# Performance work log

Hardware: AMD Instinct MI355X
Metric: run time of the kernel (lower is better)

The kernel has to match this reference:

```python
import jax, jax.numpy as jnp
import numpy as np

F_DIM = 4096
HID = 256
COR = 32
N_FRAMES = 200
NB = 30
TS = 9  # 4 + 5 time_steps


def _gru(xg, hg, wx, wh, bx, bh):
    # torch.nn.GRU cell math, gates ordered (r, z, n)
    gx = xg @ wx + bx
    gh = hg @ wh + bh
    xr, xz, xn = jnp.split(gx, 3, axis=-1)
    hr, hz, hn = jnp.split(gh, 3, axis=-1)
    r = jax.nn.sigmoid(xr + hr)
    z = jax.nn.sigmoid(xz + hz)
    n = jnp.tanh(xn + r * hn)
    return (1.0 - z) * n + z * hg


def _sattn(h, mask):
    # parameter-free scaled dot-product attention across active tracks
    d = jnp.asarray(h.shape[-1], h.dtype)
    s = (h @ h.T) / jnp.sqrt(d)
    s = jnp.where(mask[None, :], s, -1e9)
    a = jax.nn.softmax(s, axis=-1)
    out = a @ h
    return jnp.where(mask[:, None], out, h)


def setup_inputs() -> dict:
    key = jax.random.key(0)
    ks = jax.random.split(key, 20)
    flow = jax.random.normal(ks[0], (1, N_FRAMES, NB + 1, F_DIM), jnp.float32)
    x = jax.random.normal(ks[1], (1, N_FRAMES, NB + 1, F_DIM), jnp.float32)
    # y: [track_id, x1,y1,x2,y2, label, conf, d0..d5] -> 13 channels
    track = jnp.broadcast_to(jnp.arange(1, NB + 1, dtype=jnp.float32)[None, None, :, None], (1, N_FRAMES, NB, 1))
    coords = jax.random.uniform(ks[2], (1, N_FRAMES, NB, 4), jnp.float32, 0.0, 1000.0)
    label = jnp.round(jax.random.uniform(ks[3], (1, N_FRAMES, NB, 1), jnp.float32))
    conf = jax.random.uniform(ks[4], (1, N_FRAMES, NB, 1), jnp.float32)
    dist = jax.random.normal(ks[5], (1, N_FRAMES, NB, 6), jnp.float32)
    y = jnp.concatenate([track, coords, label, conf, dist], axis=-1)
    toa = jnp.ones((1, 1), jnp.float32)
    s = 0.02
    p = lambda k, shp: s * jax.random.normal(k, shp, jnp.float32)
    return {
        "x": x, "y": y, "toa": toa, "flow": flow,
        "W_rgb": p(ks[6], (F_DIM, HID)), "b_rgb": jnp.zeros((HID,), jnp.float32),
        "W_bb": p(ks[7], (5, HID)), "b_bb": jnp.zeros((HID,), jnp.float32),
        "W_dd": p(ks[8], (6, HID)), "b_dd": jnp.zeros((HID,), jnp.float32),
        "W_proj": p(ks[9], (HID, COR)), "b_proj": jnp.zeros((COR,), jnp.float32),
        "Wx_c": p(ks[10], (COR, 3 * COR)), "Wh_c": p(ks[11], (COR, 3 * COR)),
        "bx_c": jnp.zeros((3 * COR,), jnp.float32), "bh_c": jnp.zeros((3 * COR,), jnp.float32),
        "Wx_g": p(ks[12], (2 * HID, 3 * HID)), "Wh_g": p(ks[13], (HID, 3 * HID)),
        "bx_g": jnp.zeros((3 * HID,), jnp.float32), "bh_g": jnp.zeros((3 * HID,), jnp.float32),
        "W_out": p(ks[14], (2 * HID + COR, 1)), "b_out": jnp.zeros((1,), jnp.float32),
        "W_pbox": p(ks[15], (2 * HID + COR, 4 * TS)), "b_pbox": jnp.zeros((4 * TS,), jnp.float32),
    }


def reference(x, y, toa, flow, W_rgb, b_rgb, W_bb, b_bb, W_dd, b_dd, W_proj, b_proj,
              Wx_c, Wh_c, bx_c, bh_c, Wx_g, Wh_g, bx_g, bh_g, W_out, b_out, W_pbox, b_pbox):
    T = x.shape[1] - TS
    norm = jnp.array([1920.0, 1200.0, 1920.0, 1200.0], y.dtype)
    nb = y[0, :, :, 1:5] / norm                      # (N, 30, 4) normalized boxes
    # future targets: 9 future frames of normalized boxes, flattened -> (T, 30, 36)
    fut = jnp.concatenate([nb[1 + i:1 + i + T] for i in range(TS)], axis=-1)
    flow_f = flow[0, :T]                             # (T, 31, F)
    yf = y[0, :T]                                    # (T, 30, 13)
    nbf = nb[:T]
    act = yf[..., 0] != 0                            # (T, 30) active-track mask

    def step(carry, inp):
        h, hc, bacc, oacc = carry
        ft, yt, nbt, futt, at = inp
        atf = at.astype(h.dtype)
        rgb = jax.nn.relu(ft @ W_rgb + b_rgb)        # (31, H)
        img = jnp.broadcast_to(rgb[0], (NB, rgb.shape[-1]))
        comb = jnp.concatenate([rgb[1:], img], axis=-1)            # (30, 2H)
        bfeat = jax.nn.relu(jnp.concatenate([nbt, yt[:, 6:7]], axis=-1) @ W_bb + b_bb)
        dfeat = jax.nn.relu(yt[:, 7:13] @ W_dd + b_dd)
        xc = dfeat @ W_proj + b_proj
        hc_n = _gru(xc, hc, Wx_c, Wh_c, bx_c, bh_c)  # CorGRU, output_cor = hidden
        h_n = _gru(comb, h, Wx_g, Wh_g, bx_g, bh_g)
        feat = jnp.concatenate([h_n, bfeat, hc_n], axis=-1)        # (30, 2H+32)
        logit = (feat @ W_out + b_out)[:, 0]
        pbox = feat @ W_pbox + b_pbox                # (30, 36)
        d = pbox - futt
        ad = jnp.abs(d)
        sl1 = jnp.mean(jnp.where(ad < 1.0, 0.5 * d * d, ad - 0.5), axis=-1)  # SmoothL1 per box
        bacc = bacc + jnp.sum(sl1 * atf)
        tgt = yt[:, 5]
        bce = jnp.maximum(logit, 0.0) - logit * tgt + jnp.log1p(jnp.exp(-jnp.abs(logit)))
        oacc = oacc + 0.05 * jnp.sum(bce * atf)
        h2 = jnp.where(at[:, None], h_n, h)
        hc2 = jnp.where(at[:, None], hc_n, hc)
        return (_sattn(h2, at), _sattn(hc2, at), bacc, oacc), None

    init = (jnp.zeros((NB, HID), flow.dtype), jnp.zeros((NB, COR), flow.dtype),
            jnp.zeros((), flow.dtype), jnp.zeros((), flow.dtype))
    (h, hc, bbox_l, obj_l), _ = jax.lax.scan(step, init, (flow_f, yf, nbf, fut, act))
    total = obj_l + bbox_l + 0.3 * bbox_l            # object + bbox + inter(0.3*bbox)
    return total
```

## Files before the change

kernel.cpp:

```cpp
#include <hip/hip_runtime.h>
#include <math.h>
#include <stdint.h>

#define T_STEPS 191
#define NB1 31
#define YS 13
#define NBLK 8

typedef short bf8 __attribute__((ext_vector_type(8)));
typedef float f16x __attribute__((ext_vector_type(16)));

#define MFMA32 __builtin_amdgcn_mfma_f32_32x32x16_bf16

__device__ __forceinline__ float sigmoid_(float x) { return 1.f / (1.f + expf(-x)); }

__device__ __forceinline__ unsigned bf16b(float x){
  unsigned u = __float_as_uint(x);
  return (u + 0x7fffu + ((u>>16)&1u)) >> 16;
}
__device__ __forceinline__ float bf16f(unsigned b){ return __uint_as_float(b<<16); }

__device__ __forceinline__ bf8 ldfrag(const unsigned short* p, int slot){
  uint4 u = *reinterpret_cast<const uint4*>(p + slot*8);
  return __builtin_bit_cast(bf8, u);
}
__device__ __forceinline__ bf8 ldg4(const unsigned* p){
  uint4 u = *reinterpret_cast<const uint4*>(p);
  return __builtin_bit_cast(bf8, u);
}
__device__ __forceinline__ bf8 gather8(const unsigned short* fr, int base){
  unsigned w0 = (unsigned)fr[base]    | ((unsigned)fr[base+8]<<16);
  unsigned w1 = (unsigned)fr[base+16] | ((unsigned)fr[base+24]<<16);
  unsigned w2 = (unsigned)fr[base+32] | ((unsigned)fr[base+40]<<16);
  unsigned w3 = (unsigned)fr[base+48] | ((unsigned)fr[base+56]<<16);
  uint4 u; u.x=w0; u.y=w1; u.z=w2; u.w=w3;
  return __builtin_bit_cast(bf8, u);
}
__device__ __forceinline__ f16x zf16(){
  f16x v;
#pragma unroll
  for (int q=0;q<16;++q) v[q]=0.f;
  return v;
}
__device__ __forceinline__ int aslot(int m, int k){
  return ((k>>4)*64 + m + ((k>>3)&1)*32)*8 + (k&7);
}

__device__ __forceinline__ void store_dw_mall_f(float* p, float v) {
    asm volatile("global_store_dword %0, %1, off sc0 sc1"
                 :: "v"((uintptr_t)p), "v"(v) : "memory");
}
__device__ __forceinline__ void store_dw_mall_u(unsigned* p, unsigned v) {
    asm volatile("global_store_dword %0, %1, off sc0 sc1"
                 :: "v"((uintptr_t)p), "v"(v) : "memory");
}
__device__ __forceinline__ void atomic_inc_mall(unsigned* p) {
    asm volatile("global_atomic_add %0, %1, off sc1"
                 :: "v"((uintptr_t)p), "v"(1u) : "memory");
}
__device__ __forceinline__ unsigned load_u32_mall(const unsigned* p) {
    unsigned v;
    asm volatile("global_load_dword %0, %1, off sc0 sc1\n\ts_waitcnt vmcnt(0)"
                 : "=v"(v) : "v"((uintptr_t)p) : "memory");
    return v;
}

template <bool GATHER, bool RELU>
__global__ __launch_bounds__(256) void gemm_tiled(
    const float* __restrict__ A, const float* __restrict__ B,
    const float* __restrict__ bias, float* __restrict__ C,
    int M, int N, int K)
{
    __shared__ float As[16][65];
    __shared__ float Bs[16][65];
    const int tid = threadIdx.x;
    const int tm = tid >> 4, tn = tid & 15;
    const int rowBase = blockIdx.y * 64;
    const int colBase = blockIdx.x * 64;
    float acc[4][4] = {};
    for (int kt = 0; kt < K; kt += 16) {
        #pragma unroll
        for (int l = 0; l < 4; ++l) {
            const int idx = tid + l * 256;
            const int kk = idx & 15, rr = idx >> 4;
            const int row = rowBase + rr;
            float v = 0.f;
            if (row < M) {
                if (GATHER) {
                    const int t = row / 30, i = row - t * 30;
                    const int k = kt + kk;
                    const int src = (k < 256) ? ((t * NB1 + i + 1) * 256 + k)
                                              : (t * NB1 * 256 + (k - 256));
                    v = A[src];
                } else {
                    v = A[(size_t)row * K + kt + kk];
                }
            }
            As[kk][rr] = v;
            const int nn = idx & 63, k2 = idx >> 6;
            Bs[k2][nn] = B[(size_t)(kt + k2) * N + colBase + nn];
        }
        __syncthreads();
        #pragma unroll
        for (int kk = 0; kk < 16; ++kk) {
            float a[4], b[4];
            #pragma unroll
            for (int i = 0; i < 4; ++i) a[i] = As[kk][tm * 4 + i];
            #pragma unroll
            for (int j = 0; j < 4; ++j) b[j] = Bs[kk][tn * 4 + j];
            #pragma unroll
            for (int i = 0; i < 4; ++i)
                #pragma unroll
                for (int j = 0; j < 4; ++j)
                    acc[i][j] = fmaf(a[i], b[j], acc[i][j]);
        }
        __syncthreads();
    }
    #pragma unroll
    for (int i = 0; i < 4; ++i) {
        const int row = rowBase + tm * 4 + i;
        if (row < M) {
            #pragma unroll
            for (int j = 0; j < 4; ++j) {
                const int col = colBase + tn * 4 + j;
                float v = acc[i][j] + bias[col];
                if (RELU) v = fmaxf(v, 0.f);
                C[(size_t)row * N + col] = v;
            }
        }
    }
}

__global__ __launch_bounds__(256) void prep_wg(const float* __restrict__ Whg,
                                               unsigned* __restrict__ wpg)
{
    const int idx = blockIdx.x * 256 + threadIdx.x;
    const int j  = idx & 3;
    const int l  = (idx >> 2) & 63;
    const int kb = (idx >> 8) & 15;
    const int nt = idx >> 12;
    const int g = nt / 3, gate = nt - g * 3;
    const int col = gate * 256 + g * 32 + (l & 31);
    const int k2 = kb * 8 + ((l >> 5) << 2) + j;
    const unsigned lo = bf16b(Whg[(size_t)(2 * k2) * 768 + col]);
    const unsigned hi = bf16b(Whg[(size_t)(2 * k2 + 1) * 768 + col]);
    wpg[idx] = lo | (hi << 16);
}

__global__ __launch_bounds__(256) void prep_hd(const float* __restrict__ Wpbox,
                                               const float* __restrict__ Wout,
                                               unsigned* __restrict__ hdh,
                                               unsigned* __restrict__ hdl)
{
    const int idx = blockIdx.x * 256 + threadIdx.x;
    if (idx >= 9216) return;
    const int j = idx & 3;
    const int l = (idx >> 2) & 63;
    const int kbnt = idx >> 8;
    const int kb = kbnt % 18, nt = kbnt / 18;
    const int d = nt * 32 + (l & 31);
    const int k0 = kb * 16 + ((l >> 5) << 3) + 2 * j;
    float v0 = 0.f, v1 = 0.f;
    if (d < 37) {
        const int r0 = (k0 < 256) ? k0 : 512 + (k0 - 256);
        const int r1 = (k0 + 1 < 256) ? (k0 + 1) : 512 + (k0 + 1 - 256);
        v0 = (d < 36) ? Wpbox[(size_t)r0 * 36 + d] : Wout[r0];
        v1 = (d < 36) ? Wpbox[(size_t)r1 * 36 + d] : Wout[r1];
    }
    const unsigned h0 = bf16b(v0), h1 = bf16b(v1);
    const unsigned l0 = bf16b(v0 - bf16f(h0)), l1 = bf16b(v1 - bf16f(h1));
    hdh[idx] = h0 | (h1 << 16);
    hdl[idx] = l0 | (l1 << 16);
}

__global__ __launch_bounds__(256) void prep_hcw(const float* __restrict__ Whc,
                                                unsigned* __restrict__ hch,
                                                unsigned* __restrict__ hcl)
{
    const int idx = blockIdx.x * 256 + threadIdx.x;
    if (idx >= 1536) return;
    const int j = idx & 3;
    const int l = (idx >> 2) & 63;
    const int kb = (idx >> 8) & 1;
    const int nt = idx >> 9;
    const int col = nt * 32 + (l & 31);
    const int k0 = kb * 16 + ((l >> 5) << 3) + 2 * j;
    const float v0 = Whc[k0 * 96 + col];
    const float v1 = Whc[(k0 + 1) * 96 + col];
    const unsigned h0 = bf16b(v0), h1 = bf16b(v1);
    const unsigned l0 = bf16b(v0 - bf16f(h0)), l1 = bf16b(v1 - bf16f(h1));
    hch[idx] = h0 | (h1 << 16);
    hcl[idx] = l0 | (l1 << 16);
}

__global__ void prep_bias(const float* __restrict__ bxg, const float* __restrict__ bhg,
                          const float* __restrict__ bxc, const float* __restrict__ bhc,
                          float* __restrict__ biasg, float* __restrict__ biasc)
{
    const int t = threadIdx.x;
    if (t < 768) biasg[t] = bxg[t] + (t < 512 ? bhg[t] : 0.f);
    if (t < 96)  biasc[t] = bxc[t] + (t < 64 ? bhc[t] : 0.f);
}

__global__ __launch_bounds__(256) void precomp_kernel(
    const float* __restrict__ y,
    const float* __restrict__ Wbb, const float* __restrict__ bbb,
    const float* __restrict__ Wdd, const float* __restrict__ bdd,
    const float* __restrict__ Wproj, const float* __restrict__ bproj,
    const float* __restrict__ Wxc, const float* __restrict__ biasc,
    const float* __restrict__ Wpbox, const float* __restrict__ bpbox,
    const float* __restrict__ Wout, const float* __restrict__ bout,
    float* __restrict__ gxc, float* __restrict__ pbox_b, float* __restrict__ logit_b)
{
    const int m = blockIdx.x;
    const int tid = threadIdx.x;
    __shared__ float bf[256], df[256], xcs[32], yl[16];
    if (tid < YS) yl[tid] = y[m * YS + tid];
    __syncthreads();
    const float invnorm[4] = {1.f/1920.f, 1.f/1200.f, 1.f/1920.f, 1.f/1200.f};
    {
        float s = bbb[tid];
        s = fmaf(yl[1] * invnorm[0], Wbb[0 * 256 + tid], s);
        s = fmaf(yl[2] * invnorm[1], Wbb[1 * 256 + tid], s);
        s = fmaf(yl[3] * invnorm[2], Wbb[2 * 256 + tid], s);
        s = fmaf(yl[4] * invnorm[3], Wbb[3 * 256 + tid], s);
        s = fmaf(yl[6],              Wbb[4 * 256 + tid], s);
        bf[tid] = fmaxf(s, 0.f);
    }
    {
        float s = bdd[tid];
        #pragma unroll
        for (int k = 0; k < 6; ++k) s = fmaf(yl[7 + k], Wdd[k * 256 + tid], s);
        df[tid] = fmaxf(s, 0.f);
    }
    __syncthreads();
    {
        const int c = tid >> 3, p = tid & 7;
        float s = 0.f;
        for (int k = p; k < 256; k += 8) s = fmaf(df[k], Wproj[k * 32 + c], s);
        s += __shfl_xor(s, 1); s += __shfl_xor(s, 2); s += __shfl_xor(s, 4);
        if (p == 0) xcs[c] = s + bproj[c];
    }
    __syncthreads();
    if (tid < 96) {
        float s = biasc[tid];
        #pragma unroll
        for (int k = 0; k < 32; ++k) s = fmaf(xcs[k], Wxc[k * 96 + tid], s);
        gxc[m * 96 + tid] = s;
    }
    {
        const int d = tid >> 2, p = tid & 3;
        if (d < 37) {
            float s = 0.f;
            if (d < 36) {
                for (int k = p; k < 256; k += 4) s = fmaf(bf[k], Wpbox[(256 + k) * 36 + d], s);
            } else {
                for (int k = p; k < 256; k += 4) s = fmaf(bf[k], Wout[256 + k], s);
            }
            s += __shfl_xor(s, 1); s += __shfl_xor(s, 2);
            if (p == 0) {
                if (d < 36) pbox_b[m * 36 + d] = s + bpbox[d];
                else        logit_b[m] = s + bout[0];
            }
        }
    }
}

__global__ __launch_bounds__(512, 2) void seq8(
    const float* __restrict__ y,
    const float* __restrict__ gxg,
    const float* __restrict__ gxc,
    const float* __restrict__ pbox_b,
    const float* __restrict__ logit_b,
    const unsigned* __restrict__ wpg,
    const unsigned* __restrict__ hdh, const unsigned* __restrict__ hdl,
    const unsigned* __restrict__ hch, const unsigned* __restrict__ hcl,
    const float* __restrict__ bhg,
    const float* __restrict__ bhc,
    unsigned* __restrict__ h2x,
    float* __restrict__ pbx,
    unsigned* __restrict__ bar,
    float* __restrict__ parts)
{
    const int tid = threadIdx.x;
    const int bb = blockIdx.x;
    const int lane = tid & 63, wid = tid >> 6;
    const int half = lane >> 5, ln31 = lane & 31;

    __shared__ __align__(16) unsigned wgl[12288];
    __shared__ __align__(16) unsigned short hA_hi[8192], hA_lo[8192];
    __shared__ __align__(16) unsigned short hnf_hi[1024], hnf_lo[1024];
    __shared__ __align__(16) unsigned short cf_hi[1024],  cf_lo[1024];
    __shared__ __align__(16) unsigned short cnf_hi[1024], cnf_lo[1024];
    __shared__ __align__(16) unsigned short wf_hi[1024],  wf_lo[1024];
    __shared__ __align__(16) unsigned short cwf_hi[1024], cwf_lo[1024];
    __shared__ float exch[6144];
    __shared__ float gxgs[2880];
    __shared__ float gxcs[2880];
    __shared__ float hcst[1056];
    __shared__ float actf[32], bhnl[32], bhcl[32], red[16];

    {
        const unsigned* wsrc = wpg + (size_t)(3 * bb) * 4096;
        for (int i = tid; i < 12288; i += 512) wgl[i] = wsrc[i];
    }
    for (int i = tid; i < 8192; i += 512){ hA_hi[i] = 0; hA_lo[i] = 0; }
    for (int i = tid; i < 1024; i += 512){
        hnf_hi[i]=0; hnf_lo[i]=0; cf_hi[i]=0; cf_lo[i]=0;
        cnf_hi[i]=0; cnf_lo[i]=0; wf_hi[i]=0; wf_lo[i]=0;
        cwf_hi[i]=0; cwf_lo[i]=0;
    }
    for (int i = tid; i < 1056; i += 512) hcst[i] = 0.f;
    if (tid < 32){ bhnl[tid] = bhg[512 + bb*32 + tid]; bhcl[tid] = bhc[64 + tid]; }
    float bacc = 0.f, oacc = 0.f;
    __syncthreads();

    for (int t = 0; t < T_STEPS; ++t) {
        const int m0 = t * 30;
        const int dbuf = t & 1;
        unsigned* h2b = h2x + dbuf * 8192;
        float* pbb = pbx + dbuf * 9600;

        float4 sg0, sg1, sc0v, sc1v;
        const bool hasg = (tid < 360);
        if (hasg){
            { const int i = tid;       const int obj = i/24, r24 = i - obj*24;
              sg0 = *(const float4*)(gxg + (size_t)(m0+obj)*768 + (r24>>3)*256 + bb*32 + (r24&7)*4); }
            { const int i = tid + 360; const int obj = i/24, r24 = i - obj*24;
              sg1 = *(const float4*)(gxg + (size_t)(m0+obj)*768 + (r24>>3)*256 + bb*32 + (r24&7)*4); }
        }
        const bool hasc = (bb == 7) && (tid < 360);
        if (hasc){
            { const int i = tid;       const int obj = i/24, c4 = i - obj*24;
              sc0v = *(const float4*)(gxc + (size_t)(m0+obj)*96 + c4*4); }
            { const int i = tid + 360; const int obj = i/24, c4 = i - obj*24;
              sc1v = *(const float4*)(gxc + (size_t)(m0+obj)*96 + c4*4); }
        }
        if (tid < 32) actf[tid] = (tid < 30 && y[(size_t)(m0+tid)*YS] != 0.f) ? 1.f : 0.f;

        if (wid < 3){
            f16x acc = zf16();
            const unsigned* wb = wgl + wid * 4096;
#pragma unroll 4
            for (int kb = 0; kb < 16; ++kb){
                const bf8 bw = ldg4(wb + (kb*64 + lane)*4);
                const bf8 ah = ldfrag(hA_hi, kb*64 + lane);
                const bf8 al = ldfrag(hA_lo, kb*64 + lane);
                acc = MFMA32(ah, bw, acc, 0,0,0);
                acc = MFMA32(al, bw, acc, 0,0,0);
            }
#pragma unroll
            for (int q = 0; q < 16; ++q){
                const int row = (q&3) + ((q>>2)<<3) + (half<<2);
                exch[wid*1024 + row*32 + ln31] = acc[q];
            }
        } else if (wid < 6 && bb == 7){
            const int g3 = wid - 3;
            f16x acc = zf16();
#pragma unroll
            for (int kb = 0; kb < 2; ++kb){
                const bf8 ah = ldfrag(cf_hi, kb*64 + lane);
                const bf8 al = ldfrag(cf_lo, kb*64 + lane);
                const bf8 wh = ldg4(hch + ((g3*2 + kb)*64 + lane)*4);
                const bf8 wl = ldg4(hcl + ((g3*2 + kb)*64 + lane)*4);
                acc = MFMA32(ah, wh, acc, 0,0,0);
                acc = MFMA32(ah, wl, acc, 0,0,0);
                acc = MFMA32(al, wh, acc, 0,0,0);
            }
#pragma unroll
            for (int q = 0; q < 16; ++q){
                const int row = (q&3) + ((q>>2)<<3) + (half<<2);
                exch[(3+g3)*1024 + row*32 + ln31] = acc[q];
            }
        }
        if (hasg){
            { const int i = tid;       const int obj = i/24, r24 = i - obj*24;
              *(float4*)(gxgs + obj*96 + r24*4) = sg0; }
            { const int i = tid + 360; const int obj = i/24, r24 = i - obj*24;
              *(float4*)(gxgs + obj*96 + r24*4) = sg1; }
        }
        if (hasc){
            { const int i = tid;       const int obj = i/24, c4 = i - obj*24;
              *(float4*)(gxcs + obj*96 + c4*4) = sc0v; }
            { const int i = tid + 360; const int obj = i/24, c4 = i - obj*24;
              *(float4*)(gxcs + obj*96 + c4*4) = sc1v; }
        }
        __syncthreads();

        if (tid < 480){
#pragma unroll
            for (int s = 0; s < 2; ++s){
                const int e = tid*2 + s;
                const int obj = e >> 5, dim = e & 31;
                const float rv = sigmoid_(exch[obj*32 + dim]        + gxgs[obj*96 + dim]);
                const float zv = sigmoid_(exch[1024 + obj*32 + dim] + gxgs[obj*96 + 32 + dim]);
                const float nv = tanhf(gxgs[obj*96 + 64 + dim]
                                       + rv*(exch[2048 + obj*32 + dim] + bhnl[dim]));
                const int sl = aslot(obj, bb*32 + dim);
                const float h = bf16f(hA_hi[sl]) + bf16f(hA_lo[sl]);
                const float hnv = (1.f - zv)*nv + zv*h;
                const float h2 = (actf[obj] > 0.f) ? hnv : h;
                const unsigned hb = bf16b(h2), lb = bf16b(h2 - bf16f(hb));
                store_dw_mall_u(h2b + sl, hb | (lb << 16));
                const int sl2 = aslot(obj, dim);
                const unsigned nh = bf16b(hnv), nl = bf16b(hnv - bf16f(nh));
                hnf_hi[sl2] = (unsigned short)nh; hnf_lo[sl2] = (unsigned short)nl;
            }
            if (bb == 7){
#pragma unroll
                for (int s = 0; s < 2; ++s){
                    const int e = tid*2 + s;
                    const int obj = e >> 5, cd = e & 31;
                    const float rv = sigmoid_(exch[3072 + obj*32 + cd] + gxcs[obj*96 + cd]);
                    const float zv = sigmoid_(exch[4096 + obj*32 + cd] + gxcs[obj*96 + 32 + cd]);
                    const float nv = tanhf(gxcs[obj*96 + 64 + cd]
                                           + rv*(exch[5120 + obj*32 + cd] + bhcl[cd]));
                    const float hc = hcst[obj*33 + cd];
                    const float cnv = (1.f - zv)*nv + zv*hc;
                    const float c2 = (actf[obj] > 0.f) ? cnv : hc;
                    hcst[obj*33 + cd] = c2;
                    const int sl2 = aslot(obj, cd);
                    const unsigned hb = bf16b(c2), lb = bf16b(c2 - bf16f(hb));
                    cf_hi[sl2] = (unsigned short)hb; cf_lo[sl2] = (unsigned short)lb;
                    const unsigned nh = bf16b(cnv), nl = bf16b(cnv - bf16f(nh));
                    cnf_hi[sl2] = (unsigned short)nh; cnf_lo[sl2] = (unsigned short)nl;
                }
            }
        }
        __syncthreads();

        if (wid < 2){
            f16x hp = zf16();
#pragma unroll
            for (int kb = 0; kb < 2; ++kb){
                const bf8 ah = ldfrag(hnf_hi, kb*64 + lane);
                const bf8 al = ldfrag(hnf_lo, kb*64 + lane);
                const int kbg = 2*bb + kb;
                const bf8 wh = ldg4(hdh + ((wid*18 + kbg)*64 + lane)*4);
                const bf8 wl = ldg4(hdl + ((wid*18 + kbg)*64 + lane)*4);
                hp = MFMA32(ah, wh, hp, 0,0,0);
                hp = MFMA32(al, wh, hp, 0,0,0);
                hp = MFMA32(ah, wl, hp, 0,0,0);
            }
            if (bb == 7){
#pragma unroll
                for (int kb = 0; kb < 2; ++kb){
                    const bf8 ah = ldfrag(cnf_hi, kb*64 + lane);
                    const bf8 al = ldfrag(cnf_lo, kb*64 + lane);
                    const bf8 wh = ldg4(hdh + ((wid*18 + 16 + kb)*64 + lane)*4);
                    const bf8 wl = ldg4(hdl + ((wid*18 + 16 + kb)*64 + lane)*4);
                    hp = MFMA32(ah, wh, hp, 0,0,0);
                    hp = MFMA32(al, wh, hp, 0,0,0);
                    hp = MFMA32(ah, wl, hp, 0,0,0);
                }
            }
            const int d = wid*32 + ln31;
            if (d < 37){
#pragma unroll
                for (int q = 0; q < 16; ++q){
                    const int obj = (q&3) + ((q>>2)<<3) + (half<<2);
                    if (obj < 30) store_dw_mall_f(pbb + (obj*40 + d)*8 + bb, hp[q]);
                }
            }
        }

        asm volatile("s_waitcnt vmcnt(0)" ::: "memory");
        __syncthreads();
        if (tid == 0){
            atomic_inc_mall(bar);
            const unsigned tgtc = (unsigned)(NBLK * (t + 1));
            unsigned cur;
            do { asm volatile("s_sleep 1" :::); cur = load_u32_mall(bar); } while (cur < tgtc);
        }
        __syncthreads();

        {
            const int nOb = (bb == 7) ? 2 : 4;
            if (tid < nOb * 37){
                const int oo = tid / 37, d = tid - oo*37;
                const int obj = bb*4 + oo;
                if (actf[obj] > 0.f){
                    const float* pp = pbb + (obj*40 + d)*8;
                    float4 f0, f1;
                    asm volatile("global_load_dwordx4 %0, %2, off sc0 sc1\n\t"
                                 "global_load_dwordx4 %1, %3, off sc0 sc1\n\t"
                                 "s_waitcnt vmcnt(0)"
                                 : "=v"(f0), "=v"(f1)
                                 : "v"((uintptr_t)pp), "v"((uintptr_t)(pp+4)) : "memory");
                    const float sum8 = f0.x+f0.y+f0.z+f0.w + f1.x+f1.y+f1.z+f1.w;
                    const int m = m0 + obj;
                    if (d < 36){
                        const int s4 = d >> 2, cc = d & 3;
                        const float fn = (cc & 1) ? (1.f/1200.f) : (1.f/1920.f);
                        const float fu = y[(size_t)((t+1+s4)*30 + obj)*YS + 1 + cc] * fn;
                        const float df = sum8 + pbox_b[(size_t)m*36 + d] - fu;
                        const float ad = fabsf(df);
                        bacc += ((ad < 1.f) ? 0.5f*df*df : ad - 0.5f) * (1.f/36.f);
                    } else {
                        const float l = sum8 + logit_b[m];
                        const float tg = y[(size_t)m*YS + 5];
                        oacc += 0.05f * (fmaxf(l, 0.f) - l*tg + log1pf(expf(-fabsf(l))));
                    }
                }
            }
        }
        {
            unsigned uu[16];
#pragma unroll
            for (int j = 0; j < 16; ++j){
                const unsigned* sp = h2b + tid + j*512;
                asm volatile("global_load_dword %0, %1, off sc0 sc1"
                             : "=v"(uu[j]) : "v"((uintptr_t)sp) : "memory");
            }
            asm volatile("s_waitcnt vmcnt(0)" ::: "memory");
#pragma unroll
            for (int j = 0; j < 16; ++j){
                const int idx = tid + j*512;
                hA_hi[idx] = (unsigned short)(uu[j] & 0xffffu);
                hA_lo[idx] = (unsigned short)(uu[j] >> 16);
            }
        }
        __syncthreads();

        if (wid < 3){
            f16x s = zf16();
#pragma unroll 4
            for (int kb = 0; kb < 16; ++kb){
                const bf8 ah = ldfrag(hA_hi, kb*64 + lane);
                const bf8 al = ldfrag(hA_lo, kb*64 + lane);
                if (wid == 0)      s = MFMA32(ah, ah, s, 0,0,0);
                else if (wid == 1) s = MFMA32(ah, al, s, 0,0,0);
                else               s = MFMA32(al, ah, s, 0,0,0);
            }
#pragma unroll
            for (int q = 0; q < 16; ++q){
                const int row = (q&3) + ((q>>2)<<3) + (half<<2);
                exch[wid*1024 + row*32 + ln31] = s[q];
            }
        } else if (wid == 3 && bb == 7){
            f16x s = zf16();
#pragma unroll
            for (int kb = 0; kb < 2; ++kb){
                const bf8 ah = ldfrag(cf_hi, kb*64 + lane);
                const bf8 al = ldfrag(cf_lo, kb*64 + lane);
                s = MFMA32(ah, ah, s, 0,0,0);
                s = MFMA32(ah, al, s, 0,0,0);
                s = MFMA32(al, ah, s, 0,0,0);
            }
#pragma unroll
            for (int q = 0; q < 16; ++q){
                const int row = (q&3) + ((q>>2)<<3) + (half<<2);
                exch[3072 + row*32 + ln31] = s[q];
            }
        }
        __syncthreads();

        if (wid == 0 && lane < 30){
            float sv[30]; float mx = -1e30f;
#pragma unroll
            for (int j = 0; j < 30; ++j){
                float x = exch[lane*32 + j] + exch[1024 + lane*32 + j] + exch[2048 + lane*32 + j];
                x = (actf[j] > 0.f) ? x * 0.0625f : -1e9f;
                sv[j] = x; mx = fmaxf(mx, x);
            }
            float sum = 0.f;
#pragma unroll
            for (int j = 0; j < 30; ++j){ sv[j] = expf(sv[j] - mx); sum += sv[j]; }
            const float inv = 1.f / sum;
#pragma unroll
            for (int j = 0; j < 32; ++j){
                const float w = (j < 30) ? sv[j]*inv : 0.f;
                const unsigned hb = bf16b(w), lb = bf16b(w - bf16f(hb));
                const int sl = aslot(lane, j);
                wf_hi[sl] = (unsigned short)hb; wf_lo[sl] = (unsigned short)lb;
            }
        } else if (wid == 1 && bb == 7 && lane < 30){
            float sv[30]; float mx = -1e30f;
#pragma unroll
            for (int j = 0; j < 30; ++j){
                float x = exch[3072 + lane*32 + j];
                x = (actf[j] > 0.f) ? x * 0.17677669529663687f : -1e9f;
                sv[j] = x; mx = fmaxf(mx, x);
            }
            float sum = 0.f;
#pragma unroll
            for (int j = 0; j < 30; ++j){ sv[j] = expf(sv[j] - mx); sum += sv[j]; }
            const float inv = 1.f / sum;
#pragma unroll
            for (int j = 0; j < 32; ++j){
                const float w = (j < 30) ? sv[j]*inv : 0.f;
                const unsigned hb = bf16b(w), lb = bf16b(w - bf16f(hb));
                const int sl = aslot(lane, j);
                cwf_hi[sl] = (unsigned short)hb; cwf_lo[sl] = (unsigned short)lb;
            }
        }
        __syncthreads();

        {
            const int dd = wid*32 + ln31;
            f16x ao = zf16();
#pragma unroll
            for (int kb2 = 0; kb2 < 2; ++kb2){
                const bf8 wh = ldfrag(wf_hi, kb2*64 + lane);
                const bf8 wl = ldfrag(wf_lo, kb2*64 + lane);
                const int base = ((dd>>4)*64 + kb2*16 + (half<<3) + ((dd>>3)&1)*32)*8 + (dd&7);
                const bf8 bh = gather8(hA_hi, base);
                const bf8 bl = gather8(hA_lo, base);
                ao = MFMA32(wh, bh, ao, 0,0,0);
                ao = MFMA32(wh, bl, ao, 0,0,0);
                ao = MFMA32(wl, bh, ao, 0,0,0);
            }
#pragma unroll
            for (int q = 0; q < 16; ++q){
                const int obj = (q&3) + ((q>>2)<<3) + (half<<2);
                const int sl = aslot(obj, dd);
                const float h2v = bf16f(hA_hi[sl]) + bf16f(hA_lo[sl]);
                const float v = (actf[obj] > 0.f) ? ao[q] : h2v;
                const unsigned hb = bf16b(v), lb = bf16b(v - bf16f(hb));
                hA_hi[sl] = (unsigned short)hb; hA_lo[sl] = (unsigned short)lb;
            }
        }
        if (bb == 7 && wid == 0){
            f16x co = zf16();
#pragma unroll
            for (int kb2 = 0; kb2 < 2; ++kb2){
                const bf8 wh = ldfrag(cwf_hi, kb2*64 + lane);
                const bf8 wl = ldfrag(cwf_lo, kb2*64 + lane);
                const int base = ((ln31>>4)*64 + kb2*16 + (half<<3) + ((ln31>>3)&1)*32)*8 + (ln31&7);
                const bf8 bh = gather8(cf_hi, base);
                const bf8 bl = gather8(cf_lo, base);
                co = MFMA32(wh, bh, co, 0,0,0);
                co = MFMA32(wh, bl, co, 0,0,0);
                co = MFMA32(wl, bh, co, 0,0,0);
            }
#pragma unroll
            for (int q = 0; q < 16; ++q){
                const int obj = (q&3) + ((q>>2)<<3) + (half<<2);
                const float c2v = hcst[obj*33 + ln31];
                const float v = (actf[obj] > 0.f) ? co[q] : c2v;
                hcst[obj*33 + ln31] = v;
                const int sl = aslot(obj, ln31);
                const unsigned hb = bf16b(v), lb = bf16b(v - bf16f(hb));
                cf_hi[sl] = (unsigned short)hb; cf_lo[sl] = (unsigned short)lb;
            }
        }
        __syncthreads();
    }

#pragma unroll
    for (int o = 1; o < 64; o <<= 1){ bacc += __shfl_xor(bacc, o); oacc += __shfl_xor(oacc, o); }
    if (lane == 0){ red[wid] = bacc; red[8 + wid] = oacc; }
    __syncthreads();
    if (tid == 0){
        float b = 0.f, o = 0.f;
        for (int i = 0; i < 8; ++i){ b += red[i]; o += red[8 + i]; }
        parts[bb] = b; parts[8 + bb] = o;
    }
}

__global__ void reduce_kernel(const float* __restrict__ parts, float* __restrict__ out) {
    if (threadIdx.x == 0) {
        float b = 0.f, o = 0.f;
        for (int i = 0; i < NBLK; ++i) { b += parts[i]; o += parts[8 + i]; }
        out[0] = o + 1.3f * b;
    }
}

extern "C" void kernel_launch(void* const* d_in, const int* in_sizes, int n_in,
                              void* d_out, int out_size, void* d_ws, size_t ws_size,
                              hipStream_t stream) {
    (void)in_sizes; (void)n_in; (void)out_size; (void)ws_size;
    const float* y      = (const float*)d_in[1];
    const float* flow   = (const float*)d_in[3];
    const float* W_rgb  = (const float*)d_in[4];
    const float* b_rgb  = (const float*)d_in[5];
    const float* W_bb   = (const float*)d_in[6];
    const float* b_bb   = (const float*)d_in[7];
    const float* W_dd   = (const float*)d_in[8];
    const float* b_dd   = (const float*)d_in[9];
    const float* W_proj = (const float*)d_in[10];
    const float* b_proj = (const float*)d_in[11];
    const float* Wx_c   = (const float*)d_in[12];
    const float* Wh_c   = (const float*)d_in[13];
    const float* bx_c   = (const float*)d_in[14];
    const float* bh_c   = (const float*)d_in[15];
    const float* Wx_g   = (const float*)d_in[16];
    const float* Wh_g   = (const float*)d_in[17];
    const float* bx_g   = (const float*)d_in[18];
    const float* bh_g   = (const float*)d_in[19];
    const float* W_out  = (const float*)d_in[20];
    const float* b_out  = (const float*)d_in[21];
    const float* W_pbox = (const float*)d_in[22];
    const float* b_pbox = (const float*)d_in[23];
    float* out = (float*)d_out;

    char* ws = (char*)d_ws;
    unsigned* bar = (unsigned*)ws;
    unsigned* h2x = (unsigned*)(ws + 256);
    float* pbx    = (float*)(ws + 256 + 65536);
    float* parts  = (float*)(ws + 256 + 65536 + 76800);
    float* base   = (float*)(ws + 256 + 65536 + 76800 + 64);
    size_t off = 0;
    float* rgb    = base + off; off += (size_t)5921 * 256;
    float* gxg    = base + off; off += (size_t)5730 * 768;
    float* gxc    = base + off; off += (size_t)5730 * 96;
    float* pboxb  = base + off; off += (size_t)5730 * 36;
    float* logitb = base + off; off += 5760;
    float* biasg  = base + off; off += 768;
    float* biasc  = base + off; off += 96;
    unsigned* wpg = (unsigned*)(base + off); off += 98304;
    unsigned* hdh = (unsigned*)(base + off); off += 9216;
    unsigned* hdl = (unsigned*)(base + off); off += 9216;
    unsigned* hch = (unsigned*)(base + off); off += 1536;
    unsigned* hcl = (unsigned*)(base + off); off += 1536;

    (void)hipMemsetAsync(d_ws, 0, 256 + 65536, stream);

    prep_bias<<<1, 768, 0, stream>>>(bx_g, bh_g, bx_c, bh_c, biasg, biasc);
    prep_wg<<<384, 256, 0, stream>>>(Wh_g, wpg);
    prep_hd<<<36, 256, 0, stream>>>(W_pbox, W_out, hdh, hdl);
    prep_hcw<<<6, 256, 0, stream>>>(Wh_c, hch, hcl);

    gemm_tiled<false, true><<<dim3(4, 93), 256, 0, stream>>>(flow, W_rgb, b_rgb, rgb, 5921, 256, 4096);
    gemm_tiled<true, false><<<dim3(12, 90), 256, 0, stream>>>(rgb, Wx_g, biasg, gxg, 5730, 768, 512);
    precomp_kernel<<<5730, 256, 0, stream>>>(y, W_bb, b_bb, W_dd, b_dd, W_proj, b_proj,
                                             Wx_c, biasc, W_pbox, b_pbox, W_out, b_out,
                                             gxc, pboxb, logitb);
    seq8<<<NBLK, 512, 0, stream>>>(y, gxg, gxc, pboxb, logitb, wpg, hdh, hdl, hch, hcl,
                                   bh_g, bh_c, h2x, pbx, bar, parts);
    reduce_kernel<<<1, 64, 0, stream>>>(parts, out);
}
```

Before: 4.662 ms.

## Collapse 8-block recurrent kernel into single workgroup, drop global grid barrier

New measurement: 8.103 ms. +73.8%, slower.

```diff
diff --git a/kernel.cpp b/kernel.cpp
--- a/kernel.cpp
+++ b/kernel.cpp
@@ -5,7 +5,6 @@
 #define T_STEPS 191
 #define NB1 31
 #define YS 13
-#define NBLK 8
 
 typedef short bf8 __attribute__((ext_vector_type(8)));
 typedef float f16x __attribute__((ext_vector_type(16)));
@@ -44,25 +43,6 @@
 }
 __device__ __forceinline__ int aslot(int m, int k){
   return ((k>>4)*64 + m + ((k>>3)&1)*32)*8 + (k&7);
-}
-
-__device__ __forceinline__ void store_dw_mall_f(float* p, float v) {
-    asm volatile("global_store_dword %0, %1, off sc0 sc1"
-                 :: "v"((uintptr_t)p), "v"(v) : "memory");
-}
-__device__ __forceinline__ void store_dw_mall_u(unsigned* p, unsigned v) {
-    asm volatile("global_store_dword %0, %1, off sc0 sc1"
-                 :: "v"((uintptr_t)p), "v"(v) : "memory");
-}
-__device__ __forceinline__ void atomic_inc_mall(unsigned* p) {
-    asm volatile("global_atomic_add %0, %1, off sc1"
-                 :: "v"((uintptr_t)p), "v"(1u) : "memory");
-}
-__device__ __forceinline__ unsigned load_u32_mall(const unsigned* p) {
-    unsigned v;
-    asm volatile("global_load_dword %0, %1, off sc0 sc1\n\ts_waitcnt vmcnt(0)"
-                 : "=v"(v) : "v"((uintptr_t)p) : "memory");
-    return v;
 }
 
 template <bool GATHER, bool RELU>
@@ -266,7 +246,7 @@
     }
 }
 
-__global__ __launch_bounds__(512, 2) void seq8(
+__global__ __launch_bounds__(512, 1) void seq1(
     const float* __restrict__ y,
     const float* __restrict__ gxg,
     const float* __restrict__ gxc,
@@ -277,247 +257,146 @@
     const unsigned* __restrict__ hch, const unsigned* __restrict__ hcl,
     const float* __restrict__ bhg,
     const float* __restrict__ bhc,
-    unsigned* __restrict__ h2x,
-    float* __restrict__ pbx,
-    unsigned* __restrict__ bar,
-    float* __restrict__ parts)
+    float* __restrict__ out)
 {
     const int tid = threadIdx.x;
-    const int bb = blockIdx.x;
     const int lane = tid & 63, wid = tid >> 6;
     const int half = lane >> 5, ln31 = lane & 31;
-
-    __shared__ __align__(16) unsigned wgl[12288];
+    const int dd = wid * 32 + ln31;
+
     __shared__ __align__(16) unsigned short hA_hi[8192], hA_lo[8192];
-    __shared__ __align__(16) unsigned short hnf_hi[1024], hnf_lo[1024];
     __shared__ __align__(16) unsigned short cf_hi[1024],  cf_lo[1024];
-    __shared__ __align__(16) unsigned short cnf_hi[1024], cnf_lo[1024];
     __shared__ __align__(16) unsigned short wf_hi[1024],  wf_lo[1024];
     __shared__ __align__(16) unsigned short cwf_hi[1024], cwf_lo[1024];
-    __shared__ float exch[6144];
-    __shared__ float gxgs[2880];
-    __shared__ float gxcs[2880];
-    __shared__ float hcst[1056];
-    __shared__ float actf[32], bhnl[32], bhcl[32], red[16];
-
-    {
-        const unsigned* wsrc = wpg + (size_t)(3 * bb) * 4096;
-        for (int i = tid; i < 12288; i += 512) wgl[i] = wsrc[i];
-    }
+    __shared__ float exch[4096];
+    __shared__ float pbl[1280];
+    __shared__ float actf[32], red[16];
+
     for (int i = tid; i < 8192; i += 512){ hA_hi[i] = 0; hA_lo[i] = 0; }
     for (int i = tid; i < 1024; i += 512){
-        hnf_hi[i]=0; hnf_lo[i]=0; cf_hi[i]=0; cf_lo[i]=0;
-        cnf_hi[i]=0; cnf_lo[i]=0; wf_hi[i]=0; wf_lo[i]=0;
-        cwf_hi[i]=0; cwf_lo[i]=0;
-    }
-    for (int i = tid; i < 1056; i += 512) hcst[i] = 0.f;
-    if (tid < 32){ bhnl[tid] = bhg[512 + bb*32 + tid]; bhcl[tid] = bhc[64 + tid]; }
+        cf_hi[i]=0; cf_lo[i]=0; wf_hi[i]=0; wf_lo[i]=0; cwf_hi[i]=0; cwf_lo[i]=0;
+    }
+    const float bnd = bhg[512 + dd];
+    const float bnc = bhc[64 + ln31];
+
+    float hreg[16], hcreg[16];
+#pragma unroll
+    for (int q = 0; q < 16; ++q){ hreg[q] = 0.f; hcreg[q] = 0.f; }
     float bacc = 0.f, oacc = 0.f;
+
+    int lobj[3], ldc[3]; bool lval[3];
+#pragma unroll
+    for (int r3 = 0; r3 < 3; ++r3){
+        const int c = (tid - 128) + 384 * r3;
+        lval[r3] = (wid >= 2) && (c >= 0) && (c < 1110);
+        const int cc2 = lval[r3] ? c : 0;
+        lobj[r3] = cc2 / 37; ldc[r3] = cc2 - lobj[r3] * 37;
+    }
     __syncthreads();
 
-    for (int t = 0; t < T_STEPS; ++t) {
+    for (int t = 0; t < T_STEPS; ++t){
         const int m0 = t * 30;
-        const int dbuf = t & 1;
-        unsigned* h2b = h2x + dbuf * 8192;
-        float* pbb = pbx + dbuf * 9600;
-
-        float4 sg0, sg1, sc0v, sc1v;
-        const bool hasg = (tid < 360);
-        if (hasg){
-            { const int i = tid;       const int obj = i/24, r24 = i - obj*24;
-              sg0 = *(const float4*)(gxg + (size_t)(m0+obj)*768 + (r24>>3)*256 + bb*32 + (r24&7)*4); }
-            { const int i = tid + 360; const int obj = i/24, r24 = i - obj*24;
-              sg1 = *(const float4*)(gxg + (size_t)(m0+obj)*768 + (r24>>3)*256 + bb*32 + (r24&7)*4); }
-        }
-        const bool hasc = (bb == 7) && (tid < 360);
-        if (hasc){
-            { const int i = tid;       const int obj = i/24, c4 = i - obj*24;
-              sc0v = *(const float4*)(gxc + (size_t)(m0+obj)*96 + c4*4); }
-            { const int i = tid + 360; const int obj = i/24, c4 = i - obj*24;
-              sc1v = *(const float4*)(gxc + (size_t)(m0+obj)*96 + c4*4); }
-        }
-        if (tid < 32) actf[tid] = (tid < 30 && y[(size_t)(m0+tid)*YS] != 0.f) ? 1.f : 0.f;
-
-        if (wid < 3){
-            f16x acc = zf16();
-            const unsigned* wb = wgl + wid * 4096;
+
+        if (tid < 32) actf[tid] = (tid < 30 && y[(size_t)(m0 + tid) * YS] != 0.f) ? 1.f : 0.f;
+        float gr[16], gz[16], gn[16];
+#pragma unroll
+        for (int q = 0; q < 16; ++q){
+            const int obj = (q&3) + ((q>>2)<<3) + (half<<2);
+            if (obj < 30){
+                const float* gp = gxg + (size_t)(m0 + obj) * 768 + dd;
+                gr[q] = gp[0]; gz[q] = gp[256]; gn[q] = gp[512];
+            } else { gr[q] = 0.f; gz[q] = 0.f; gn[q] = 0.f; }
+        }
+        float pfu[3], ppb[3]; float ptg = 0.f;
+#pragma unroll
+        for (int r3 = 0; r3 < 3; ++r3){
+            pfu[r3] = 0.f; ppb[r3] = 0.f;
+            if (lval[r3]){
+                const int obj = lobj[r3], d = ldc[r3];
+                const int m = m0 + obj;
+                if (d < 36){
+                    const int s4 = d >> 2, cc = d & 3;
+                    const float fn = (cc & 1) ? (1.f/1200.f) : (1.f/1920.f);
+                    pfu[r3] = y[(size_t)((t + 1 + s4)*30 + obj)*YS + 1 + cc] * fn;
+                    ppb[r3] = pbox_b[(size_t)m*36 + d];
+                } else {
+                    ppb[r3] = logit_b[m];
+                    ptg = y[(size_t)m*YS + 5];
+                }
+            }
+        }
+
+        f16x aR = zf16(), aZ = zf16(), aN = zf16();
+        {
+            const unsigned* bRp = wpg + ((size_t)((wid*3 + 0)*16)*64 + lane)*4;
+            const unsigned* bZp = wpg + ((size_t)((wid*3 + 1)*16)*64 + lane)*4;
+            const unsigned* bNp = wpg + ((size_t)((wid*3 + 2)*16)*64 + lane)*4;
 #pragma unroll 4
             for (int kb = 0; kb < 16; ++kb){
-                const bf8 bw = ldg4(wb + (kb*64 + lane)*4);
+                const bf8 br = ldg4(bRp + kb*256);
+                const bf8 bz = ldg4(bZp + kb*256);
+                const bf8 bn = ldg4(bNp + kb*256);
                 const bf8 ah = ldfrag(hA_hi, kb*64 + lane);
                 const bf8 al = ldfrag(hA_lo, kb*64 + lane);
-                acc = MFMA32(ah, bw, acc, 0,0,0);
-                acc = MFMA32(al, bw, acc, 0,0,0);
-            }
-#pragma unroll
-            for (int q = 0; q < 16; ++q){
-                const int row = (q&3) + ((q>>2)<<3) + (half<<2);
-                exch[wid*1024 + row*32 + ln31] = acc[q];
-            }
-        } else if (wid < 6 && bb == 7){
+                aR = MFMA32(ah, br, aR, 0,0,0); aR = MFMA32(al, br, aR, 0,0,0);
+                aZ = MFMA32(ah, bz, aZ, 0,0,0); aZ = MFMA32(al, bz, aZ, 0,0,0);
+                aN = MFMA32(ah, bn, aN, 0,0,0); aN = MFMA32(al, bn, aN, 0,0,0);
+            }
+        }
+        if (wid >= 3 && wid < 6){
             const int g3 = wid - 3;
-            f16x acc = zf16();
+            f16x cacc = zf16();
 #pragma unroll
             for (int kb = 0; kb < 2; ++kb){
                 const bf8 ah = ldfrag(cf_hi, kb*64 + lane);
                 const bf8 al = ldfrag(cf_lo, kb*64 + lane);
                 const bf8 wh = ldg4(hch + ((g3*2 + kb)*64 + lane)*4);
                 const bf8 wl = ldg4(hcl + ((g3*2 + kb)*64 + lane)*4);
-                acc = MFMA32(ah, wh, acc, 0,0,0);
-                acc = MFMA32(ah, wl, acc, 0,0,0);
-                acc = MFMA32(al, wh, acc, 0,0,0);
+                cacc = MFMA32(ah, wh, cacc, 0,0,0);
+                cacc = MFMA32(ah, wl, cacc, 0,0,0);
+                cacc = MFMA32(al, wh, cacc, 0,0,0);
             }
 #pragma unroll
             for (int q = 0; q < 16; ++q){
                 const int row = (q&3) + ((q>>2)<<3) + (half<<2);
-                exch[(3+g3)*1024 + row*32 + ln31] = acc[q];
-            }
-        }
-        if (hasg){
-            { const int i = tid;       const int obj = i/24, r24 = i - obj*24;
-              *(float4*)(gxgs + obj*96 + r24*4) = sg0; }
-            { const int i = tid + 360; const int obj = i/24, r24 = i - obj*24;
-              *(float4*)(gxgs + obj*96 + r24*4) = sg1; }
-        }
-        if (hasc){
-            { const int i = tid;       const int obj = i/24, c4 = i - obj*24;
-              *(float4*)(gxcs + obj*96 + c4*4) = sc0v; }
-            { const int i = tid + 360; const int obj = i/24, c4 = i - obj*24;
-              *(float4*)(gxcs + obj*96 + c4*4) = sc1v; }
+                exch[g3*1024 + row*32 + ln31] = cacc[q];
+            }
         }
         __syncthreads();
 
-        if (tid < 480){
-#pragma unroll
-            for (int s = 0; s < 2; ++s){
-                const int e = tid*2 + s;
-                const int obj = e >> 5, dim = e & 31;
-                const float rv = sigmoid_(exch[obj*32 + dim]        + gxgs[obj*96 + dim]);
-                const float zv = sigmoid_(exch[1024 + obj*32 + dim] + gxgs[obj*96 + 32 + dim]);
-                const float nv = tanhf(gxgs[obj*96 + 64 + dim]
-                                       + rv*(exch[2048 + obj*32 + dim] + bhnl[dim]));
-                const int sl = aslot(obj, bb*32 + dim);
-                const float h = bf16f(hA_hi[sl]) + bf16f(hA_lo[sl]);
-                const float hnv = (1.f - zv)*nv + zv*h;
-                const float h2 = (actf[obj] > 0.f) ? hnv : h;
-                const unsigned hb = bf16b(h2), lb = bf16b(h2 - bf16f(hb));
-                store_dw_mall_u(h2b + sl, hb | (lb << 16));
-                const int sl2 = aslot(obj, dim);
-                const unsigned nh = bf16b(hnv), nl = bf16b(hnv - bf16f(nh));
-                hnf_hi[sl2] = (unsigned short)nh; hnf_lo[sl2] = (unsigned short)nl;
-            }
-            if (bb == 7){
-#pragma unroll
-                for (int s = 0; s < 2; ++s){
-                    const int e = tid*2 + s;
-                    const int obj = e >> 5, cd = e & 31;
-                    const float rv = sigmoid_(exch[3072 + obj*32 + cd] + gxcs[obj*96 + cd]);
-                    const float zv = sigmoid_(exch[4096 + obj*32 + cd] + gxcs[obj*96 + 32 + cd]);
-                    const float nv = tanhf(gxcs[obj*96 + 64 + cd]
-                                           + rv*(exch[5120 + obj*32 + cd] + bhcl[cd]));
-                    const float hc = hcst[obj*33 + cd];
-                    const float cnv = (1.f - zv)*nv + zv*hc;
-                    const float c2 = (actf[obj] > 0.f) ? cnv : hc;
-                    hcst[obj*33 + cd] = c2;
-                    const int sl2 = aslot(obj, cd);
-                    const unsigned hb = bf16b(c2), lb = bf16b(c2 - bf16f(hb));
-                    cf_hi[sl2] = (unsigned short)hb; cf_lo[sl2] = (unsigned short)lb;
-                    const unsigned nh = bf16b(cnv), nl = bf16b(cnv - bf16f(nh));
-                    cnf_hi[sl2] = (unsigned short)nh; cnf_lo[sl2] = (unsigned short)nl;
-                }
-            }
-        }
-        __syncthreads();
-
-        if (wid < 2){
-            f16x hp = zf16();
-#pragma unroll
-            for (int kb = 0; kb < 2; ++kb){
-                const bf8 ah = ldfrag(hnf_hi, kb*64 + lane);
-                const bf8 al = ldfrag(hnf_lo, kb*64 + lane);
-                const int kbg = 2*bb + kb;
-                const bf8 wh = ldg4(hdh + ((wid*18 + kbg)*64 + lane)*4);
-                const bf8 wl = ldg4(hdl + ((wid*18 + kbg)*64 + lane)*4);
-                hp = MFMA32(ah, wh, hp, 0,0,0);
-                hp = MFMA32(al, wh, hp, 0,0,0);
-                hp = MFMA32(ah, wl, hp, 0,0,0);
-            }
-            if (bb == 7){
-#pragma unroll
-                for (int kb = 0; kb < 2; ++kb){
-                    const bf8 ah = ldfrag(cnf_hi, kb*64 + lane);
-                    const bf8 al = ldfrag(cnf_lo, kb*64 + lane);
-                    const bf8 wh = ldg4(hdh + ((wid*18 + 16 + kb)*64 + lane)*4);
-                    const bf8 wl = ldg4(hdl + ((wid*18 + 16 + kb)*64 + lane)*4);
-                    hp = MFMA32(ah, wh, hp, 0,0,0);
-                    hp = MFMA32(al, wh, hp, 0,0,0);
-                    hp = MFMA32(ah, wl, hp, 0,0,0);
-                }
-            }
-            const int d = wid*32 + ln31;
-            if (d < 37){
-#pragma unroll
-                for (int q = 0; q < 16; ++q){
-                    const int obj = (q&3) + ((q>>2)<<3) + (half<<2);
-                    if (obj < 30) store_dw_mall_f(pbb + (obj*40 + d)*8 + bb, hp[q]);
-                }
-            }
-        }
-
-        asm volatile("s_waitcnt vmcnt(0)" ::: "memory");
-        __syncthreads();
-        if (tid == 0){
-            atomic_inc_mall(bar);
-            const unsigned tgtc = (unsigned)(NBLK * (t + 1));
-            unsigned cur;
-            do { asm volatile("s_sleep 1" :::); cur = load_u32_mall(bar); } while (cur < tgtc);
-        }
-        __syncthreads();
-
-        {
-            const int nOb = (bb == 7) ? 2 : 4;
-            if (tid < nOb * 37){
-                const int oo = tid / 37, d = tid - oo*37;
-                const int obj = bb*4 + oo;
-                if (actf[obj] > 0.f){
-                    const float* pp = pbb + (obj*40 + d)*8;
-                    float4 f0, f1;
-                    asm volatile("global_load_dwordx4 %0, %2, off sc0 sc1\n\t"
-                                 "global_load_dwordx4 %1, %3, off sc0 sc1\n\t"
-                                 "s_waitcnt vmcnt(0)"
-                                 : "=v"(f0), "=v"(f1)
-                                 : "v"((uintptr_t)pp), "v"((uintptr_t)(pp+4)) : "memory");
-                    const float sum8 = f0.x+f0.y+f0.z+f0.w + f1.x+f1.y+f1.z+f1.w;
-                    const int m = m0 + obj;
-                    if (d < 36){
-                        const int s4 = d >> 2, cc = d & 3;
-                        const float fn = (cc & 1) ? (1.f/1200.f) : (1.f/1920.f);
-                        const float fu = y[(size_t)((t+1+s4)*30 + obj)*YS + 1 + cc] * fn;
-                        const float df = sum8 + pbox_b[(size_t)m*36 + d] - fu;
-                        const float ad = fabsf(df);
-                        bacc += ((ad < 1.f) ? 0.5f*df*df : ad - 0.5f) * (1.f/36.f);
-                    } else {
-                        const float l = sum8 + logit_b[m];
-                        const float tg = y[(size_t)m*YS + 5];
-                        oacc += 0.05f * (fmaxf(l, 0.f) - l*tg + log1pf(expf(-fabsf(l))));
-                    }
-                }
-            }
-        }
-        {
-            unsigned uu[16];
-#pragma unroll
-            for (int j = 0; j < 16; ++j){
-                const unsigned* sp = h2b + tid + j*512;
-                asm volatile("global_load_dword %0, %1, off sc0 sc1"
-                             : "=v"(uu[j]) : "v"((uintptr_t)sp) : "memory");
-            }
-            asm volatile("s_waitcnt vmcnt(0)" ::: "memory");
-#pragma unroll
-            for (int j = 0; j < 16; ++j){
-                const int idx = tid + j*512;
-                hA_hi[idx] = (unsigned short)(uu[j] & 0xffffu);
-                hA_lo[idx] = (unsigned short)(uu[j] >> 16);
+#pragma unroll
+        for (int q = 0; q < 16; ++q){
+            const int obj = (q&3) + ((q>>2)<<3) + (half<<2);
+            const float rv = sigmoid_(aR[q] + gr[q]);
+            const float zv = sigmoid_(aZ[q] + gz[q]);
+            const float nv = tanhf(gn[q] + rv*(aN[q] + bnd));
+            const float hv = hreg[q];
+            const float hnv = (1.f - zv)*nv + zv*hv;
+            const float h2 = (actf[obj] > 0.f) ? hnv : hv;
+            hreg[q] = h2;
+            const int sl = aslot(obj, dd);
+            const unsigned hb = bf16b(h2), lb = bf16b(h2 - bf16f(hb));
+            hA_hi[sl] = (unsigned short)hb; hA_lo[sl] = (unsigned short)lb;
+        }
+        if (wid == 7){
+#pragma unroll
+            for (int q = 0; q < 16; ++q){
+                const int obj = (q&3) + ((q>>2)<<3) + (half<<2);
+                float xr = 0.f, xz = 0.f, xn = 0.f;
+                if (obj < 30){
+                    const float* gp = gxc + (size_t)(m0 + obj)*96 + ln31;
+                    xr = gp[0]; xz = gp[32]; xn = gp[64];
+                }
+                const float rv = sigmoid_(exch[obj*32 + ln31] + xr);
+                const float zv = sigmoid_(exch[1024 + obj*32 + ln31] + xz);
+                const float nv = tanhf(xn + rv*(exch[2048 + obj*32 + ln31] + bnc));
+                const float hcv = hcreg[q];
+                const float cnv = (1.f - zv)*nv + zv*hcv;
+                const float c2 = (actf[obj] > 0.f) ? cnv : hcv;
+                hcreg[q] = c2;
+                const int sl = aslot(obj, ln31);
+                const unsigned hb = bf16b(c2), lb = bf16b(c2 - bf16f(hb));
+                cf_hi[sl] = (unsigned short)hb; cf_lo[sl] = (unsigned short)lb;
             }
         }
         __syncthreads();
@@ -537,7 +416,38 @@
                 const int row = (q&3) + ((q>>2)<<3) + (half<<2);
                 exch[wid*1024 + row*32 + ln31] = s[q];
             }
-        } else if (wid == 3 && bb == 7){
+        } else if (wid < 5){
+            const int nt = wid - 3;
+            f16x h1 = zf16(), h2v = zf16(), h3 = zf16();
+#pragma unroll 4
+            for (int kb = 0; kb < 16; ++kb){
+                const bf8 ah = ldfrag(hA_hi, kb*64 + lane);
+                const bf8 al = ldfrag(hA_lo, kb*64 + lane);
+                const bf8 wh = ldg4(hdh + ((nt*18 + kb)*64 + lane)*4);
+                const bf8 wl = ldg4(hdl + ((nt*18 + kb)*64 + lane)*4);
+                h1 = MFMA32(ah, wh, h1, 0,0,0);
+                h2v = MFMA32(al, wh, h2v, 0,0,0);
+                h3 = MFMA32(ah, wl, h3, 0,0,0);
+            }
+#pragma unroll
+            for (int kb = 16; kb < 18; ++kb){
+                const bf8 ah = ldfrag(cf_hi, (kb-16)*64 + lane);
+                const bf8 al = ldfrag(cf_lo, (kb-16)*64 + lane);
+                const bf8 wh = ldg4(hdh + ((nt*18 + kb)*64 + lane)*4);
+                const bf8 wl = ldg4(hdl + ((nt*18 + kb)*64 + lane)*4);
+                h1 = MFMA32(ah, wh, h1, 0,0,0);
+                h2v = MFMA32(al, wh, h2v, 0,0,0);
+                h3 = MFMA32(ah, wl, h3, 0,0,0);
+            }
+            const int d = nt*32 + ln31;
+            if (d < 37){
+#pragma unroll
+                for (int q = 0; q < 16; ++q){
+                    const int obj = (q&3) + ((q>>2)<<3) + (half<<2);
+                    if (obj < 30) pbl[obj*40 + d] = h1[q] + h2v[q] + h3[q];
+                }
+            }
+        } else if (wid == 5){
             f16x s = zf16();
 #pragma unroll
             for (int kb = 0; kb < 2; ++kb){
@@ -555,49 +465,69 @@
         }
         __syncthreads();
 
-        if (wid == 0 && lane < 30){
-            float sv[30]; float mx = -1e30f;
-#pragma unroll
-            for (int j = 0; j < 30; ++j){
-                float x = exch[lane*32 + j] + exch[1024 + lane*32 + j] + exch[2048 + lane*32 + j];
-                x = (actf[j] > 0.f) ? x * 0.0625f : -1e9f;
-                sv[j] = x; mx = fmaxf(mx, x);
-            }
-            float sum = 0.f;
-#pragma unroll
-            for (int j = 0; j < 30; ++j){ sv[j] = expf(sv[j] - mx); sum += sv[j]; }
-            const float inv = 1.f / sum;
-#pragma unroll
-            for (int j = 0; j < 32; ++j){
-                const float w = (j < 30) ? sv[j]*inv : 0.f;
-                const unsigned hb = bf16b(w), lb = bf16b(w - bf16f(hb));
-                const int sl = aslot(lane, j);
-                wf_hi[sl] = (unsigned short)hb; wf_lo[sl] = (unsigned short)lb;
-            }
-        } else if (wid == 1 && bb == 7 && lane < 30){
-            float sv[30]; float mx = -1e30f;
-#pragma unroll
-            for (int j = 0; j < 30; ++j){
-                float x = exch[3072 + lane*32 + j];
-                x = (actf[j] > 0.f) ? x * 0.17677669529663687f : -1e9f;
-                sv[j] = x; mx = fmaxf(mx, x);
-            }
-            float sum = 0.f;
-#pragma unroll
-            for (int j = 0; j < 30; ++j){ sv[j] = expf(sv[j] - mx); sum += sv[j]; }
-            const float inv = 1.f / sum;
-#pragma unroll
-            for (int j = 0; j < 32; ++j){
-                const float w = (j < 30) ? sv[j]*inv : 0.f;
-                const unsigned hb = bf16b(w), lb = bf16b(w - bf16f(hb));
-                const int sl = aslot(lane, j);
-                cwf_hi[sl] = (unsigned short)hb; cwf_lo[sl] = (unsigned short)lb;
+        if (wid == 0){
+            if (lane < 30){
+                float sv[30]; float mx = -1e30f;
+#pragma unroll
+                for (int j = 0; j < 30; ++j){
+                    float x = exch[lane*32 + j] + exch[1024 + lane*32 + j] + exch[2048 + lane*32 + j];
+                    x = (actf[j] > 0.f) ? x * 0.0625f : -1e9f;
+                    sv[j] = x; mx = fmaxf(mx, x);
+                }
+                float sum = 0.f;
+#pragma unroll
+                for (int j = 0; j < 30; ++j){ sv[j] = expf(sv[j] - mx); sum += sv[j]; }
+                const float inv = 1.f / sum;
+#pragma unroll
+                for (int j = 0; j < 32; ++j){
+                    const float w = (j < 30) ? sv[j]*inv : 0.f;
+                    const unsigned hb = bf16b(w), lb = bf16b(w - bf16f(hb));
+                    const int sl = aslot(lane, j);
+                    wf_hi[sl] = (unsigned short)hb; wf_lo[sl] = (unsigned short)lb;
+                }
+            }
+        } else if (wid == 1){
+            if (lane < 30){
+                float sv[30]; float mx = -1e30f;
+#pragma unroll
+                for (int j = 0; j < 30; ++j){
+                    float x = exch[3072 + lane*32 + j];
+                    x = (actf[j] > 0.f) ? x * 0.17677669529663687f : -1e9f;
+                    sv[j] = x; mx = fmaxf(mx, x);
+                }
+                float sum = 0.f;
+#pragma unroll
+                for (int j = 0; j < 30; ++j){ sv[j] = expf(sv[j] - mx); sum += sv[j]; }
+                const float inv = 1.f / sum;
+#pragma unroll
+                for (int j = 0; j < 32; ++j){
+                    const float w = (j < 30) ? sv[j]*inv : 0.f;
+                    const unsigned hb = bf16b(w), lb = bf16b(w - bf16f(hb));
+                    const int sl = aslot(lane, j);
+                    cwf_hi[sl] = (unsigned short)hb; cwf_lo[sl] = (unsigned short)lb;
+                }
+            }
+        } else {
+#pragma unroll
+            for (int r3 = 0; r3 < 3; ++r3){
+                if (lval[r3]){
+                    const int obj = lobj[r3], d = ldc[r3];
+                    if (actf[obj] > 0.f){
+                        if (d < 36){
+                            const float df = pbl[obj*40 + d] + ppb[r3] - pfu[r3];
+                            const float ad = fabsf(df);
+                            bacc += ((ad < 1.f) ? 0.5f*df*df : ad - 0.5f) * (1.f/36.f);
+                        } else {
+                            const float l = pbl[obj*40 + 36] + ppb[r3];
+                            oacc += 0.05f * (fmaxf(l, 0.f) - l*ptg + log1pf(expf(-fabsf(l))));
+                        }
+                    }
+                }
             }
         }
         __syncthreads();
 
         {
-            const int dd = wid*32 + ln31;
             f16x ao = zf16();
 #pragma unroll
             for (int kb2 = 0; kb2 < 2; ++kb2){
@@ -613,14 +543,14 @@
 #pragma unroll
             for (int q = 0; q < 16; ++q){
                 const int obj = (q&3) + ((q>>2)<<3) + (half<<2);
+                const float v = (actf[obj] > 0.f) ? ao[q] : hreg[q];
+                hreg[q] = v;
                 const int sl = aslot(obj, dd);
-                const float h2v = bf16f(hA_hi[sl]) + bf16f(hA_lo[sl]);
-                const float v = (actf[obj] > 0.f) ? ao[q] : h2v;
                 const unsigned hb = bf16b(v), lb = bf16b(v - bf16f(hb));
                 hA_hi[sl] = (unsigned short)hb; hA_lo[sl] = (unsigned short)lb;
             }
         }
-        if (bb == 7 && wid == 0){
+        if (wid == 7){
             f16x co = zf16();
 #pragma unroll
             for (int kb2 = 0; kb2 < 2; ++kb2){
@@ -636,9 +566,8 @@
 #pragma unroll
             for (int q = 0; q < 16; ++q){
                 const int obj = (q&3) + ((q>>2)<<3) + (half<<2);
-                const float c2v = hcst[obj*33 + ln31];
-                const float v = (actf[obj] > 0.f) ? co[q] : c2v;
-                hcst[obj*33 + ln31] = v;
+                const float v = (actf[obj] > 0.f) ? co[q] : hcreg[q];
+                hcreg[q] = v;
                 const int sl = aslot(obj, ln31);
                 const unsigned hb = bf16b(v), lb = bf16b(v - bf16f(hb));
                 cf_hi[sl] = (unsigned short)hb; cf_lo[sl] = (unsigned short)lb;
@@ -654,14 +583,6 @@
     if (tid == 0){
         float b = 0.f, o = 0.f;
         for (int i = 0; i < 8; ++i){ b += red[i]; o += red[8 + i]; }
-        parts[bb] = b; parts[8 + bb] = o;
-    }
-}
-
-__global__ void reduce_kernel(const float* __restrict__ parts, float* __restrict__ out) {
-    if (threadIdx.x == 0) {
-        float b = 0.f, o = 0.f;
-        for (int i = 0; i < NBLK; ++i) { b += parts[i]; o += parts[8 + i]; }
         out[0] = o + 1.3f * b;
     }
 }
@@ -694,12 +615,7 @@
     const float* b_pbox = (const float*)d_in[23];
     float* out = (float*)d_out;
 
-    char* ws = (char*)d_ws;
-    unsigned* bar = (unsigned*)ws;
-    unsigned* h2x = (unsigned*)(ws + 256);
-    float* pbx    = (float*)(ws + 256 + 65536);
-    float* parts  = (float*)(ws + 256 + 65536 + 76800);
-    float* base   = (float*)(ws + 256 + 65536 + 76800 + 64);
+    float* base = (float*)d_ws;
     size_t off = 0;
     float* rgb    = base + off; off += (size_t)5921 * 256;
     float* gxg    = base + off; off += (size_t)5730 * 768;
@@ -714,8 +630,6 @@
     unsigned* hch = (unsigned*)(base + off); off += 1536;
     unsigned* hcl = (unsigned*)(base + off); off += 1536;
 
-    (void)hipMemsetAsync(d_ws, 0, 256 + 65536, stream);
-
     prep_bias<<<1, 768, 0, stream>>>(bx_g, bh_g, bx_c, bh_c, biasg, biasc);
     prep_wg<<<384, 256, 0, stream>>>(Wh_g, wpg);
     prep_hd<<<36, 256, 0, stream>>>(W_pbox, W_out, hdh, hdl);
@@ -726,7 +640,6 @@
     precomp_kernel<<<5730, 256, 0, stream>>>(y, W_bb, b_bb, W_dd, b_dd, W_proj, b_proj,
                                              Wx_c, biasc, W_pbox, b_pbox, W_out, b_out,
                                              gxc, pboxb, logitb);
-    seq8<<<NBLK, 512, 0, stream>>>(y, gxg, gxc, pboxb, logitb, wpg, hdh, hdl, hch, hcl,
-                                   bh_g, bh_c, h2x, pbx, bar, parts);
-    reduce_kernel<<<1, 64, 0, stream>>>(parts, out);
-}
+    seq1<<<1, 512, 0, stream>>>(y, gxg, gxc, pboxb, logitb, wpg, hdh, hdl, hch, hcl,
+                                bh_g, bh_c, out);
+}
```
